# Optimization experiments

Hardware: AMD Instinct MI355X
Metric: run time of the kernel (lower is better)

## Reference

```python
import math
import jax, jax.numpy as jnp
import numpy as np

EPS = 1e-10


def setup_inputs() -> dict:
    key = jax.random.key(0)
    k1, k2, k3, k4 = jax.random.split(key, 4)
    B, R, S, C = 2, 16384, 48, 32
    colors = jax.random.uniform(k1, (B, R, S, C), dtype=jnp.float32)
    densities = jax.random.normal(k2, (B, R, S, 1), dtype=jnp.float32)
    # ray-march depths: monotonically increasing along the sample dim, in [2.0, 6.0]
    depths = jnp.sort(
        jax.random.uniform(k3, (B, R, S, 1), dtype=jnp.float32, minval=2.0, maxval=6.0),
        axis=2,
    )
    sample_coordinates = jax.random.normal(k4, (B, R, S * 3), dtype=jnp.float32)
    return {
        "colors": colors,
        "densities": densities,
        "depths": depths,
        "sample_coordinates": sample_coordinates,
    }


def reference(colors, densities, depths, sample_coordinates):
    # rendering_options: clamp_mode='softplus' (only supported mode), white_back=False
    # return_depth=True
    B, R, S, _ = colors.shape

    deltas = depths[:, :, 1:] - depths[:, :, :-1]                      # [B,R,S-1,1]
    colors_mid = (colors[:, :, :-1] + colors[:, :, 1:]) * 0.5          # [B,R,S-1,C]
    densities_mid = (densities[:, :, :-1] + densities[:, :, 1:]) * 0.5
    depths_mid = (depths[:, :, :-1] + depths[:, :, 1:]) * 0.5

    densities_mid = jax.nn.softplus(densities_mid - 1.0)

    alpha = 1.0 - jnp.exp(-densities_mid * deltas)                     # [B,R,S-1,1]
    alpha_shifted = jnp.concatenate(
        [jnp.ones_like(alpha[:, :, :1]), 1.0 - alpha + EPS], axis=2
    )
    transmittance = jnp.cumprod(alpha_shifted, axis=2)[:, :, :-1]
    weights = alpha * transmittance                                    # [B,R,S-1,1]

    composite_rgb = jnp.sum(weights * colors_mid, axis=2)              # [B,R,C]
    weight_total = jnp.sum(weights, axis=2)                            # [B,R,1]
    composite_depth = jnp.sum(weights * depths_mid, axis=2) / weight_total
    composite_depth = jnp.nan_to_num(composite_depth, nan=jnp.inf)
    composite_depth = jnp.clip(composite_depth, jnp.min(depths), jnp.max(depths))

    # return_depth branch (in-place add in torch happens AFTER rgb/depth are computed)
    weights_out = weights.at[:, :, -1].add(1.0 - weight_total)
    sc = sample_coordinates.reshape(B, R, S, 3)
    sc_mid = (sc[:, :, :-1] + sc[:, :, 1:]) * 0.5                      # [B,R,S-1,3]
    xyz = jnp.sum(weights_out * sc_mid, axis=2)                        # [B,R,3]
    img_size = int(math.sqrt(R))
    xyz = xyz.reshape(B, img_size, img_size, -1)
    weight_total_img = weight_total.reshape(B, img_size, img_size, -1)

    composite_rgb = composite_rgb * 2.0 - 1.0
    return (composite_rgb, composite_depth, weights_out, xyz, weight_total_img)
```

## Files before the change

### kernel.cpp

```cpp
#include <hip/hip_runtime.h>

#define NS   48
#define NSM1 47
#define NC   32
#define WPB  8
#define MMB  64

__launch_bounds__(256)
__global__ void depth_minmax_partials(const float* __restrict__ depths,
                                      float2* __restrict__ partials,
                                      int nrays) {
    const int tid  = threadIdx.x;
    const int lane = tid & 63;
    const int wv   = tid >> 6;
    float mn = __uint_as_float(0x7f800000u);
    float mx = -mn;
    for (int r = blockIdx.x * 256 + tid; r < nrays; r += MMB * 256) {
        mn = fminf(mn, depths[(size_t)r * NS]);
        mx = fmaxf(mx, depths[(size_t)r * NS + NSM1]);
    }
#pragma unroll
    for (int off = 32; off; off >>= 1) {
        mn = fminf(mn, __shfl_xor(mn, off));
        mx = fmaxf(mx, __shfl_xor(mx, off));
    }
    __shared__ float smn[4], smx[4];
    if (lane == 0) { smn[wv] = mn; smx[wv] = mx; }
    __syncthreads();
    if (tid == 0) {
        mn = fminf(fminf(smn[0], smn[1]), fminf(smn[2], smn[3]));
        mx = fmaxf(fmaxf(smx[0], smx[1]), fmaxf(smx[2], smx[3]));
        partials[blockIdx.x] = make_float2(mn, mx);
    }
}

__launch_bounds__(WPB * 64)
__global__ void raymarch_kernel(const float* __restrict__ colors,
                                const float* __restrict__ densities,
                                const float* __restrict__ depths,
                                const float* __restrict__ sc,
                                const float2* __restrict__ partials,
                                float* __restrict__ out_rgb,
                                float* __restrict__ out_depth,
                                float* __restrict__ out_w,
                                float* __restrict__ out_xyz,
                                float* __restrict__ out_wt,
                                int nrays) {
    __shared__ float wlds[WPB][52];
    __shared__ float scl[WPB][146];

    const int lane = threadIdx.x & 63;
    const int wv   = threadIdx.x >> 6;
    const int r    = blockIdx.x * WPB + wv;
    const bool active = (r < nrays);
    const int rr = active ? r : (nrays - 1);

    const float2 pp = partials[lane];
    const float4* colp = (const float4*)(colors + (size_t)rr * (NS * NC));
    float4 cv[6];
#pragma unroll
    for (int t = 0; t < 6; ++t) cv[t] = colp[t * 64 + lane];

    const size_t scbase = (size_t)rr * (NS * 3);
#pragma unroll
    for (int i = 0; i < 3; ++i) {
        const int idx = lane + i * 64;
        if (idx < NS * 3) scl[wv][idx] = sc[scbase + idx];
    }

    const size_t rbase = (size_t)rr * NS;
    float d = 0.0f, de = 0.0f;
    if (lane < NS) {
        d  = depths[rbase + lane];
        de = densities[rbase + lane];
    }
    const float d1  = __shfl_down(d, 1);
    const float de1 = __shfl_down(de, 1);

    float alpha = 0.0f, dmid = 0.0f, f = 1.0f;
    if (lane < NSM1) {
        const float delta = d1 - d;
        dmid = 0.5f * (d + d1);
        const float x  = 0.5f * (de + de1) - 1.0f;
        const float sp = fmaxf(x, 0.0f) + __logf(1.0f + __expf(-fabsf(x)));
        alpha = 1.0f - __expf(-sp * delta);
        f = 1.0f - alpha + 1e-10f;
    }

    float g = __shfl_up(f, 1);
    if (lane == 0) g = 1.0f;
#pragma unroll
    for (int off = 1; off < 64; off <<= 1) {
        const float v = __shfl_up(g, off);
        if (lane >= off) g *= v;
    }
    const float wgt = (lane < NSM1) ? alpha * g : 0.0f;

    float wt = wgt, dsum = wgt * dmid;
#pragma unroll
    for (int off = 32; off; off >>= 1) {
        wt   += __shfl_xor(wt, off);
        dsum += __shfl_xor(dsum, off);
    }

    if (lane < NSM1) wlds[wv][lane + 1] = wgt;
    if (lane == 0) { wlds[wv][0] = 0.0f; wlds[wv][NS] = 0.0f; }
    __syncthreads();

    const int soff = lane >> 3;
    float4 acc = make_float4(0.f, 0.f, 0.f, 0.f);
#pragma unroll
    for (int t = 0; t < 6; ++t) {
        const int j = t * 8 + soff;
        const float a = 0.5f * (wlds[wv][j] + wlds[wv][j + 1]);
        acc.x = fmaf(a, cv[t].x, acc.x);
        acc.y = fmaf(a, cv[t].y, acc.y);
        acc.z = fmaf(a, cv[t].z, acc.z);
        acc.w = fmaf(a, cv[t].w, acc.w);
    }
#pragma unroll
    for (int off = 8; off < 64; off <<= 1) {
        acc.x += __shfl_xor(acc.x, off);
        acc.y += __shfl_xor(acc.y, off);
        acc.z += __shfl_xor(acc.z, off);
        acc.w += __shfl_xor(acc.w, off);
    }
    if (active && lane < 8) {
        float4 o;
        o.x = fmaf(acc.x, 2.0f, -1.0f);
        o.y = fmaf(acc.y, 2.0f, -1.0f);
        o.z = fmaf(acc.z, 2.0f, -1.0f);
        o.w = fmaf(acc.w, 2.0f, -1.0f);
        ((float4*)out_rgb)[(size_t)r * (NC / 4) + lane] = o;
    }

    float px = 0.f, py = 0.f, pz = 0.f;
    if (lane < NSM1) {
        const float wout = wgt + ((lane == NSM1 - 1) ? (1.0f - wt) : 0.0f);
        const int b3 = 3 * lane;
        px = wout * (0.5f * (scl[wv][b3 + 0] + scl[wv][b3 + 3]));
        py = wout * (0.5f * (scl[wv][b3 + 1] + scl[wv][b3 + 4]));
        pz = wout * (0.5f * (scl[wv][b3 + 2] + scl[wv][b3 + 5]));
        if (active) out_w[(size_t)r * NSM1 + lane] = wout;
    }
#pragma unroll
    for (int off = 32; off; off >>= 1) {
        px += __shfl_xor(px, off);
        py += __shfl_xor(py, off);
        pz += __shfl_xor(pz, off);
    }

    float gmn = pp.x, gmx = pp.y;
#pragma unroll
    for (int off = 32; off; off >>= 1) {
        gmn = fminf(gmn, __shfl_xor(gmn, off));
        gmx = fmaxf(gmx, __shfl_xor(gmx, off));
    }
    if (active && lane == 0) {
        float cd = dsum / wt;
        if (!(cd == cd)) cd = gmx;
        cd = fminf(fmaxf(cd, gmn), gmx);
        out_depth[r] = cd;
        out_wt[r]    = wt;
        out_xyz[(size_t)r * 3 + 0] = px;
        out_xyz[(size_t)r * 3 + 1] = py;
        out_xyz[(size_t)r * 3 + 2] = pz;
    }
}

extern "C" void kernel_launch(void* const* d_in, const int* in_sizes, int n_in,
                              void* d_out, int out_size, void* d_ws, size_t ws_size,
                              hipStream_t stream) {
    const float* colors    = (const float*)d_in[0];
    const float* densities = (const float*)d_in[1];
    const float* depths    = (const float*)d_in[2];
    const float* sc        = (const float*)d_in[3];

    const int nrays   = in_sizes[1] / NS;
    const int nblocks = (nrays + WPB - 1) / WPB;

    float* out       = (float*)d_out;
    float* out_rgb   = out;
    float* out_depth = out_rgb + (size_t)nrays * NC;
    float* out_w     = out_depth + nrays;
    float* out_xyz   = out_w + (size_t)nrays * NSM1;
    float* out_wt    = out_xyz + (size_t)nrays * 3;

    float2* partials = (float2*)d_ws;

    hipLaunchKernelGGL(depth_minmax_partials, dim3(MMB), dim3(256), 0, stream,
                       depths, partials, nrays);
    hipLaunchKernelGGL(raymarch_kernel, dim3(nblocks), dim3(WPB * 64), 0, stream,
                       colors, densities, depths, sc, partials,
                       out_rgb, out_depth, out_w, out_xyz, out_wt, nrays);
}
```

Before: 47.44 us.

## Replace LDS staging with shuffles, add nontemporal loads/stores, shrink raymarch blocks

```diff
diff --git a/kernel.cpp b/kernel.cpp
--- a/kernel.cpp
+++ b/kernel.cpp
@@ -3,10 +3,12 @@
 #define NS   48
 #define NSM1 47
 #define NC   32
-#define WPB  8
+#define WPB  4
 #define MMB  64
 
-__launch_bounds__(256)
+typedef float f4v __attribute__((ext_vector_type(4)));
+
+__launch_bounds__(512)
 __global__ void depth_minmax_partials(const float* __restrict__ depths,
                                       float2* __restrict__ partials,
                                       int nrays) {
@@ -15,7 +17,7 @@
     const int wv   = tid >> 6;
     float mn = __uint_as_float(0x7f800000u);
     float mx = -mn;
-    for (int r = blockIdx.x * 256 + tid; r < nrays; r += MMB * 256) {
+    for (int r = blockIdx.x * 512 + tid; r < nrays; r += MMB * 512) {
         mn = fminf(mn, depths[(size_t)r * NS]);
         mx = fmaxf(mx, depths[(size_t)r * NS + NSM1]);
     }
@@ -24,13 +26,16 @@
         mn = fminf(mn, __shfl_xor(mn, off));
         mx = fmaxf(mx, __shfl_xor(mx, off));
     }
-    __shared__ float smn[4], smx[4];
+    __shared__ float smn[8], smx[8];
     if (lane == 0) { smn[wv] = mn; smx[wv] = mx; }
     __syncthreads();
     if (tid == 0) {
-        mn = fminf(fminf(smn[0], smn[1]), fminf(smn[2], smn[3]));
-        mx = fmaxf(fmaxf(smx[0], smx[1]), fmaxf(smx[2], smx[3]));
-        partials[blockIdx.x] = make_float2(mn, mx);
+#pragma unroll
+        for (int w = 1; w < 8; ++w) {
+            mn = fminf(smn[0] = fminf(smn[0], smn[w]), smn[0]);
+            smx[0] = fmaxf(smx[0], smx[w]);
+        }
+        partials[blockIdx.x] = make_float2(smn[0], smx[0]);
     }
 }
 
@@ -46,9 +51,6 @@
                                 float* __restrict__ out_xyz,
                                 float* __restrict__ out_wt,
                                 int nrays) {
-    __shared__ float wlds[WPB][52];
-    __shared__ float scl[WPB][146];
-
     const int lane = threadIdx.x & 63;
     const int wv   = threadIdx.x >> 6;
     const int r    = blockIdx.x * WPB + wv;
@@ -56,17 +58,17 @@
     const int rr = active ? r : (nrays - 1);
 
     const float2 pp = partials[lane];
-    const float4* colp = (const float4*)(colors + (size_t)rr * (NS * NC));
-    float4 cv[6];
+
+    const f4v* colp = (const f4v*)(colors + (size_t)rr * (NS * NC));
+    f4v cv[6];
 #pragma unroll
-    for (int t = 0; t < 6; ++t) cv[t] = colp[t * 64 + lane];
+    for (int t = 0; t < 6; ++t)
+        cv[t] = __builtin_nontemporal_load(colp + t * 64 + lane);
 
-    const size_t scbase = (size_t)rr * (NS * 3);
-#pragma unroll
-    for (int i = 0; i < 3; ++i) {
-        const int idx = lane + i * 64;
-        if (idx < NS * 3) scl[wv][idx] = sc[scbase + idx];
-    }
+    const float* scp = sc + (size_t)rr * (NS * 3);
+    const int b3 = (lane < NSM1) ? 3 * lane : 0;
+    const float s0 = scp[b3 + 0], s1 = scp[b3 + 1], s2 = scp[b3 + 2];
+    const float s3 = scp[b3 + 3], s4 = scp[b3 + 4], s5 = scp[b3 + 5];
 
     const size_t rbase = (size_t)rr * NS;
     float d = 0.0f, de = 0.0f;
@@ -74,6 +76,7 @@
         d  = depths[rbase + lane];
         de = densities[rbase + lane];
     }
+
     const float d1  = __shfl_down(d, 1);
     const float de1 = __shfl_down(de, 1);
 
@@ -103,20 +106,14 @@
         dsum += __shfl_xor(dsum, off);
     }
 
-    if (lane < NSM1) wlds[wv][lane + 1] = wgt;
-    if (lane == 0) { wlds[wv][0] = 0.0f; wlds[wv][NS] = 0.0f; }
-    __syncthreads();
+    const float a_full = 0.5f * (wgt + __shfl(wgt, (lane - 1) & 63));
 
     const int soff = lane >> 3;
-    float4 acc = make_float4(0.f, 0.f, 0.f, 0.f);
+    f4v acc = {0.f, 0.f, 0.f, 0.f};
 #pragma unroll
     for (int t = 0; t < 6; ++t) {
-        const int j = t * 8 + soff;
-        const float a = 0.5f * (wlds[wv][j] + wlds[wv][j + 1]);
-        acc.x = fmaf(a, cv[t].x, acc.x);
-        acc.y = fmaf(a, cv[t].y, acc.y);
-        acc.z = fmaf(a, cv[t].z, acc.z);
-        acc.w = fmaf(a, cv[t].w, acc.w);
+        const float a = __shfl(a_full, t * 8 + soff);
+        acc += a * cv[t];
     }
 #pragma unroll
     for (int off = 8; off < 64; off <<= 1) {
@@ -126,22 +123,22 @@
         acc.w += __shfl_xor(acc.w, off);
     }
     if (active && lane < 8) {
-        float4 o;
+        f4v o;
         o.x = fmaf(acc.x, 2.0f, -1.0f);
         o.y = fmaf(acc.y, 2.0f, -1.0f);
         o.z = fmaf(acc.z, 2.0f, -1.0f);
         o.w = fmaf(acc.w, 2.0f, -1.0f);
-        ((float4*)out_rgb)[(size_t)r * (NC / 4) + lane] = o;
+        __builtin_nontemporal_store(o, (f4v*)out_rgb + (size_t)r * (NC / 4) + lane);
     }
 
     float px = 0.f, py = 0.f, pz = 0.f;
     if (lane < NSM1) {
         const float wout = wgt + ((lane == NSM1 - 1) ? (1.0f - wt) : 0.0f);
-        const int b3 = 3 * lane;
-        px = wout * (0.5f * (scl[wv][b3 + 0] + scl[wv][b3 + 3]));
-        py = wout * (0.5f * (scl[wv][b3 + 1] + scl[wv][b3 + 4]));
-        pz = wout * (0.5f * (scl[wv][b3 + 2] + scl[wv][b3 + 5]));
-        if (active) out_w[(size_t)r * NSM1 + lane] = wout;
+        px = wout * (0.5f * (s0 + s3));
+        py = wout * (0.5f * (s1 + s4));
+        pz = wout * (0.5f * (s2 + s5));
+        if (active)
+            __builtin_nontemporal_store(wout, out_w + (size_t)r * NSM1 + lane);
     }
 #pragma unroll
     for (int off = 32; off; off >>= 1) {
@@ -188,7 +185,7 @@
 
     float2* partials = (float2*)d_ws;
 
-    hipLaunchKernelGGL(depth_minmax_partials, dim3(MMB), dim3(256), 0, stream,
+    hipLaunchKernelGGL(depth_minmax_partials, dim3(MMB), dim3(512), 0, stream,
                        depths, partials, nrays);
     hipLaunchKernelGGL(raymarch_kernel, dim3(nblocks), dim3(WPB * 64), 0, stream,
                        colors, densities, depths, sc, partials,
```

New measurement: 48.18 us. About the same (+1.6%).
